# Performance work log

Hardware: AMD Instinct MI355X
Metric: run time of the kernel (lower is better)

Reference implementation:

```python
import jax, jax.numpy as jnp
import numpy as np

B, N, E = 32, 196, 512      # batch, image regions, encoder_dim
D, EMB, V = 512, 512, 32000  # decoder_dim, embedding_dim, vocab
MAXLEN = 65


def setup_inputs() -> dict:
    key = jax.random.key(0)
    ks = jax.random.split(key, 16)
    s = lambda *sh: 1.0 / np.sqrt(sh[-1])
    return {
        "image_features": jax.random.normal(ks[0], (B, N, E), jnp.float32),
        "captions": jax.random.randint(ks[1], (B, MAXLEN), 0, V),
        "emb": jax.random.normal(ks[2], (V, EMB), jnp.float32) * 0.02,
        "Wh0": jax.random.normal(ks[3], (D, E), jnp.float32) * s(E),
        "bh0": jnp.zeros((D,), jnp.float32),
        "Wc0": jax.random.normal(ks[4], (D, E), jnp.float32) * s(E),
        "bc0": jnp.zeros((D,), jnp.float32),
        "Wenc": jax.random.normal(ks[5], (D, E), jnp.float32) * s(E),
        "Wdec": jax.random.normal(ks[6], (D, D), jnp.float32) * s(D),
        "v_att": jax.random.normal(ks[7], (D,), jnp.float32) * s(D),
        "W_ih": jax.random.normal(ks[8], (4 * D, EMB + E), jnp.float32) * s(EMB + E),
        "b_ih": jnp.zeros((4 * D,), jnp.float32),
        "W_hh": jax.random.normal(ks[9], (4 * D, D), jnp.float32) * s(D),
        "b_hh": jnp.zeros((4 * D,), jnp.float32),
        "Wfc": jax.random.normal(ks[10], (V, D), jnp.float32) * s(D),
        "bfc": jnp.zeros((V,), jnp.float32),
    }


def reference(image_features, captions, emb, Wh0, bh0, Wc0, bc0,
              Wenc, Wdec, v_att, W_ih, b_ih, W_hh, b_hh, Wfc, bfc):
    seq_len = captions.shape[1] - 1
    emb_caps = emb[captions]                     # [B, maxlen, EMB]
    xs = jnp.swapaxes(emb_caps[:, :seq_len], 0, 1)  # [T, B, EMB]

    feat_mean = image_features.mean(axis=1)      # [B, E]
    h0 = feat_mean @ Wh0.T + bh0                 # [B, D]
    c0 = feat_mean @ Wc0.T + bc0
    feat_proj = jnp.einsum('bne,de->bnd', image_features, Wenc)  # [B, N, D]

    def step(carry, xt):
        h, c = carry
        # Bahdanau additive attention over the N image regions
        e = jnp.einsum('bnd,d->bn', jnp.tanh(feat_proj + (h @ Wdec.T)[:, None, :]), v_att)
        alpha = jax.nn.softmax(e, axis=-1)                       # [B, N]
        ctx = jnp.einsum('bn,bne->be', alpha, image_features)    # [B, E]
        x = jnp.concatenate([xt, ctx], axis=-1)                  # [B, EMB+E]
        gates = x @ W_ih.T + b_ih + h @ W_hh.T + b_hh            # [B, 4D]
        i, f, g, o = jnp.split(gates, 4, axis=-1)
        c_new = jax.nn.sigmoid(f) * c + jax.nn.sigmoid(i) * jnp.tanh(g)
        h_new = jax.nn.sigmoid(o) * jnp.tanh(c_new)
        out = h_new @ Wfc.T + bfc                                # [B, V]
        return (h_new, c_new), (out, alpha)
    # dropout_p=0.0 -> dropout is identity (eval-mode reference)
    _, (outs, alphas) = jax.lax.scan(step, (h0, c0), xs)
    outputs = jnp.swapaxes(outs, 0, 1)            # [B, T, V]
    attention_weights = jnp.swapaxes(alphas, 0, 1)  # [B, T, N]
    return outputs, attention_weights
```

## Files before the change

kernel.cpp:

```cpp
#include <hip/hip_runtime.h>
#include <cstdint>
#include <cstddef>

typedef _Float16 half2_t __attribute__((ext_vector_type(2)));
typedef _Float16 half4_t __attribute__((ext_vector_type(4)));
typedef _Float16 half8_t __attribute__((ext_vector_type(8)));
typedef float    float4_t __attribute__((ext_vector_type(4)));

#define CAPLEN 65
#define PTLD 200

#define AT_LD(p)     __hip_atomic_load((p), __ATOMIC_RELAXED, __HIP_MEMORY_SCOPE_AGENT)
#define AT_ST(p, v)  __hip_atomic_store((p), (v), __ATOMIC_RELAXED, __HIP_MEMORY_SCOPE_AGENT)

#if defined(__has_builtin)
#if __has_builtin(__builtin_amdgcn_fdot2)
#define HAS_FDOT2 1
#endif
#endif

__device__ __forceinline__ float fdot2f(half2_t a, half2_t b, float c) {
#ifdef HAS_FDOT2
  return __builtin_amdgcn_fdot2(a, b, c, false);
#else
  return c + (float)a[0]*(float)b[0] + (float)a[1]*(float)b[1];
#endif
}

__device__ __forceinline__ float fast_tanh(float x) {
  float e = __expf(2.f*x);
  return 1.f - 2.f/(e + 1.f);
}
__device__ __forceinline__ float fast_sig(float x) {
  return 1.f/(1.f + __expf(-x));
}

#define MS_C1 65536
#define MS_C2 131072
#define MS_C3 655360
#define MS_C4 917504
#define MS_C5 5013504
#define MS_C6 5816320
#define MS_C7 6078464
#define MS_C8 6078976
#define MS_C9 6087168
#define MS_C10 6218240

__device__ __forceinline__ void cvt_quad(const float* __restrict__ s,
                                         _Float16* __restrict__ d, int q) {
  float4 v = ((const float4*)s)[q];
  half4_t h;
  h[0] = (_Float16)v.x; h[1] = (_Float16)v.y; h[2] = (_Float16)v.z; h[3] = (_Float16)v.w;
  ((half4_t*)d)[q] = h;
}

__global__ void mega_setup_k(
    const float* __restrict__ Wenc, _Float16* __restrict__ Wenc_h,
    const float* __restrict__ Wdec, _Float16* __restrict__ Wdec_h,
    const float* __restrict__ Wih,  _Float16* __restrict__ Wih_h,
    const float* __restrict__ Whh,  _Float16* __restrict__ Whh_h,
    const float* __restrict__ Wfc,  _Float16* __restrict__ Wfc_h,
    const float* __restrict__ imgf, _Float16* __restrict__ imgf_h,
    const float* __restrict__ emb,  const int* __restrict__ cap,
    _Float16* __restrict__ X_h,
    const float* __restrict__ b_ih, const float* __restrict__ b_hh,
    float* __restrict__ bsum,
    unsigned long long* __restrict__ hpub64,
    unsigned long long* __restrict__ epub64) {
  int stride = gridDim.x*blockDim.x;
  for (int i = blockIdx.x*blockDim.x + threadIdx.x; i < MS_C10; i += stride) {
    if (i < MS_C1) {
      cvt_quad(Wenc, Wenc_h, i);
    } else if (i < MS_C2) {
      cvt_quad(Wdec, Wdec_h, i - MS_C1);
    } else if (i < MS_C3) {
      cvt_quad(Wih, Wih_h, i - MS_C2);
    } else if (i < MS_C4) {
      cvt_quad(Whh, Whh_h, i - MS_C3);
    } else if (i < MS_C5) {
      cvt_quad(Wfc, Wfc_h, i - MS_C4);
    } else if (i < MS_C6) {
      cvt_quad(imgf, imgf_h, i - MS_C5);
    } else if (i < MS_C7) {
      int g = i - MS_C6;
      int row = g >> 7, q = g & 127;
      int t = row >> 5, b = row & 31;
      int tok = cap[b*CAPLEN + t];
      float4 v = ((const float4*)(emb + (size_t)tok*512))[q];
      half4_t h;
      h[0] = (_Float16)v.x; h[1] = (_Float16)v.y; h[2] = (_Float16)v.z; h[3] = (_Float16)v.w;
      *(half4_t*)(X_h + (size_t)row*512 + q*4) = h;
    } else if (i < MS_C8) {
      int q = i - MS_C7;
      float4 a = ((const float4*)b_ih)[q];
      float4 b = ((const float4*)b_hh)[q];
      float4 o; o.x = a.x+b.x; o.y = a.y+b.y; o.z = a.z+b.z; o.w = a.w+b.w;
      ((float4*)bsum)[q] = o;
    } else if (i < MS_C9) {
      hpub64[8192 + (i - MS_C8)] = ~0ull;
    } else {
      epub64[i - MS_C9] = ~0ull;
    }
  }
}

__global__ void init_state_k(const float* __restrict__ imgf,
                             const float* __restrict__ Wh0, const float* __restrict__ bh0,
                             const float* __restrict__ Wc0, const float* __restrict__ bc0,
                             float* __restrict__ c_state,
                             unsigned long long* __restrict__ hpub64) {
  __shared__ float fm[512];
  __shared__ float hsh[512];
  int b = blockIdx.x, tid = threadIdx.x;
  for (int dI = tid; dI < 512; dI += 256) {
    float s = 0.f;
    const float* p = imgf + ((size_t)b*196)*512 + dI;
    for (int n = 0; n < 196; n++) s += p[(size_t)n*512];
    fm[dI] = s * (1.f/196.f);
  }
  __syncthreads();
  for (int dI = tid; dI < 512; dI += 256) {
    const float* wh = Wh0 + (size_t)dI*512;
    const float* wc = Wc0 + (size_t)dI*512;
    float h = bh0[dI], c = bc0[dI];
    for (int k = 0; k < 512; k++) { h += fm[k]*wh[k]; c += fm[k]*wc[k]; }
    hsh[dI] = h;
    c_state[b*512 + dI] = c;
  }
  __syncthreads();
  {
    half2_t h2; h2[0] = (_Float16)hsh[2*tid]; h2[1] = (_Float16)hsh[2*tid+1];
    union { half2_t h; unsigned u; } cv; cv.h = h2;
    hpub64[(size_t)b*256 + tid] = (unsigned long long)cv.u;
  }
}

__device__ __forceinline__ void gemm_pt_body(const _Float16* __restrict__ A, int lda,
    const _Float16* __restrict__ Bimg, _Float16* __restrict__ Cpt, int mrows,
    int bx, int by, int bz, int tid) {
  const _Float16* B = Bimg + (size_t)bz*196*512;
  _Float16* C = Cpt + (size_t)bz*mrows*PTLD;
  int wave = tid >> 6, lane = tid & 63;
  int m0 = by*128 + (wave >> 1)*64;
  int n0 = bx*128 + (wave & 1)*64;
  int lr = lane & 15, quad = lane >> 4;
  float4_t acc[4][4];
  #pragma unroll
  for (int i = 0; i < 4; i++)
    #pragma unroll
    for (int j = 0; j < 4; j++)
      acc[i][j] = (float4_t){0.f, 0.f, 0.f, 0.f};
  const _Float16* Ap = A + (size_t)(m0 + lr)*lda + quad*8;
  const _Float16* Bp = B + (size_t)(n0 + lr)*512 + quad*8;
  for (int k0 = 0; k0 < 512; k0 += 32) {
    half8_t af[4], bf[4];
    #pragma unroll
    for (int i = 0; i < 4; i++) af[i] = *(const half8_t*)(Ap + (size_t)i*16*lda + k0);
    #pragma unroll
    for (int i = 0; i < 4; i++) bf[i] = *(const half8_t*)(Bp + (size_t)i*16*512 + k0);
    #pragma unroll
    for (int mi = 0; mi < 4; mi++)
      #pragma unroll
      for (int ni = 0; ni < 4; ni++)
        acc[mi][ni] = __builtin_amdgcn_mfma_f32_16x16x32_f16(af[mi], bf[ni], acc[mi][ni], 0, 0, 0);
  }
  #pragma unroll
  for (int mi = 0; mi < 4; mi++) {
    #pragma unroll
    for (int ni = 0; ni < 4; ni++) {
      int col = n0 + ni*16 + lr;
      if (col < PTLD) {
        #pragma unroll
        for (int r = 0; r < 4; r++) {
          int row = m0 + mi*16 + quad*4 + r;
          C[(size_t)row*PTLD + col] = (_Float16)acc[mi][ni][r];
        }
      }
    }
  }
}

__device__ __forceinline__ void gemm_ab0_body(const _Float16* __restrict__ A, int lda,
    const _Float16* __restrict__ B, int ldb, float* __restrict__ C, int ldc,
    const float* __restrict__ bias, int K, int bx, int by, int tid) {
  int wave = tid >> 6, lane = tid & 63;
  int m0 = by*128 + (wave >> 1)*64;
  int n0 = bx*128 + (wave & 1)*64;
  int lr = lane & 15, quad = lane >> 4;
  float4_t acc[4][4];
  #pragma unroll
  for (int i = 0; i < 4; i++)
    #pragma unroll
    for (int j = 0; j < 4; j++)
      acc[i][j] = (float4_t){0.f, 0.f, 0.f, 0.f};
  const _Float16* Ap = A + (size_t)(m0 + lr)*lda + quad*8;
  const _Float16* Bp = B + (size_t)(n0 + lr)*ldb + quad*8;
  for (int k0 = 0; k0 < K; k0 += 32) {
    half8_t af[4], bf[4];
    #pragma unroll
    for (int i = 0; i < 4; i++) af[i] = *(const half8_t*)(Ap + (size_t)i*16*lda + k0);
    #pragma unroll
    for (int i = 0; i < 4; i++) bf[i] = *(const half8_t*)(Bp + (size_t)i*16*ldb + k0);
    #pragma unroll
    for (int mi = 0; mi < 4; mi++)
      #pragma unroll
      for (int ni = 0; ni < 4; ni++)
        acc[mi][ni] = __builtin_amdgcn_mfma_f32_16x16x32_f16(af[mi], bf[ni], acc[mi][ni], 0, 0, 0);
  }
  #pragma unroll
  for (int mi = 0; mi < 4; mi++) {
    #pragma unroll
    for (int ni = 0; ni < 4; ni++) {
      int col = n0 + ni*16 + lr;
      float bv = bias[col];
      #pragma unroll
      for (int r = 0; r < 4; r++) {
        int row = m0 + mi*16 + quad*4 + r;
        C[(size_t)row*ldc + col] = acc[mi][ni][r] + bv;
      }
    }
  }
}

__global__ void __launch_bounds__(256) setup_gemms_k(
    const _Float16* __restrict__ Wenc_h, const _Float16* __restrict__ Wih_h,
    const _Float16* __restrict__ imgf_h, const _Float16* __restrict__ X_h,
    _Float16* __restrict__ fproj_T, _Float16* __restrict__ P_T,
    float* __restrict__ Xg, const float* __restrict__ bsum) {
  int bid = blockIdx.x, tid = threadIdx.x;
  if (bid < 256) {
    gemm_pt_body(Wenc_h, 512, imgf_h, fproj_T, 512, bid & 1, (bid >> 1) & 3, bid >> 3, tid);
  } else if (bid < 1280) {
    int l = bid - 256;
    gemm_pt_body(Wih_h + 512, 1024, imgf_h, P_T, 2048, l & 1, (l >> 1) & 15, l >> 5, tid);
  } else {
    int l = bid - 1280;
    gemm_ab0_body(X_h, 512, Wih_h, 1024, Xg, 2048, bsum, 512, l & 15, l >> 4, tid);
  }
}

__global__ void __launch_bounds__(512) loop_k(
    const _Float16* __restrict__ Wdec_h,
    const _Float16* __restrict__ Whh_h,
    const _Float16* __restrict__ fproj_T,
    const _Float16* __restrict__ P_T,
    const float*    __restrict__ Xg,
    const float*    __restrict__ v_att,
    const float*    __restrict__ c_init,
    unsigned long long* __restrict__ hpub64,
    unsigned long long* __restrict__ epub64,
    _Float16*       __restrict__ H_h,
    float*          __restrict__ out_alpha)
{
  __shared__ _Float16 P_lds[98*256*2];
  __shared__ _Float16 fp_lds[64*PTLD];
  __shared__ __align__(16) unsigned hl_u[256];
  __shared__ _Float16 Hbuf[64*64];
  __shared__ float abuf[25*64];
  __shared__ float vlf[64];
  __shared__ float hwf[64];
  __shared__ float ep[2][256];
  __shared__ float redA[8];
  __shared__ float redB[8];
  __shared__ float sa[256];
  __shared__ float sm2[512];
  __shared__ float hnl[64];
  int bid = blockIdx.x, tid = threadIdx.x;
  int r = bid & 7, b = bid >> 3;
  int row = tid & 255, half = tid >> 8;
  int typ = row >> 6, dl = row & 63;
  int grow = typ*512 + r*64 + dl;
  int lane = tid & 63;

  if (tid < 64) vlf[tid] = v_att[r*64 + tid];
  float c_reg = (tid < 64) ? c_init[b*512 + r*64 + tid] : 0.f;

  if (tid < 256) {
    const _Float16* pp = P_T + ((size_t)b*2048 + grow)*PTLD;
    half2_t* P2 = (half2_t*)P_lds;
    for (int k8 = 0; k8 < 24; k8++) {
      half8_t v8 = *(const half8_t*)(pp + k8*8);
      #pragma unroll
      for (int j2 = 0; j2 < 4; j2++) {
        half2_t h2; h2[0] = v8[2*j2]; h2[1] = v8[2*j2+1];
        P2[(k8*4 + j2)*256 + row] = h2;
      }
    }
    half4_t v4 = *(const half4_t*)(pp + 192);
    half2_t a2; a2[0] = v4[0]; a2[1] = v4[1];
    half2_t b2; b2[0] = v4[2]; b2[1] = v4[3];
    P2[96*256 + row] = a2;
    P2[97*256 + row] = b2;
  } else {
    for (int i = tid - 256; i < 64*25; i += 256) {
      int d = i/25, c = i - d*25;
      *(half8_t*)(fp_lds + d*PTLD + c*8) =
        *(const half8_t*)(fproj_T + ((size_t)(b*512 + r*64 + d))*PTLD + c*8);
    }
  }
  int eBase = (r < 4) ? r*25 : 100 + (r-4)*24;
  int eCnt  = (r < 4) ? 25 : 24;

  for (int t = 0; t < 64; ++t) {
    if (tid < 256) {
      const unsigned long long* hp = hpub64 + ((size_t)(t & 1)*32 + b)*256 + tid;
      unsigned long long v = AT_LD(hp);
      while ((unsigned)(v >> 32) != (unsigned)t) {
        __builtin_amdgcn_s_sleep(1);
        v = AT_LD(hp);
      }
      hl_u[tid] = (unsigned)v;
    }
    float xg = (half == 1) ? Xg[((size_t)t*32 + b)*2048 + grow] : 0.f;
    __syncthreads();
    {
      int dim = tid >> 3, s = tid & 7;
      const half8_t* wr = (const half8_t*)(Wdec_h + (size_t)(r*64 + dim)*512 + s*64);
      const half8_t* hh = ((const half8_t*)(const _Float16*)hl_u) + s*8;
      float a = 0.f;
      #pragma unroll
      for (int k8 = 0; k8 < 8; k8++) {
        half8_t w8 = wr[k8]; half8_t h8 = hh[k8];
        const half2_t* wp = (const half2_t*)&w8;
        const half2_t* hp = (const half2_t*)&h8;
        a = fdot2f(wp[0], hp[0], a);
        a = fdot2f(wp[1], hp[1], a);
        a = fdot2f(wp[2], hp[2], a);
        a = fdot2f(wp[3], hp[3], a);
      }
      a += __shfl_xor(a, 1);
      a += __shfl_xor(a, 2);
      a += __shfl_xor(a, 4);
      if (s == 0) hwf[dim] = a;
    }
    __syncthreads();
    {
      float a = 0.f;
      if (row < 196) {
        #pragma unroll 8
        for (int j = 0; j < 32; j++) {
          int dd = half*32 + j;
          a += vlf[dd] * fast_tanh((float)fp_lds[dd*PTLD + row] + hwf[dd]);
        }
      }
      ep[half][row] = a;
    }
    __syncthreads();
    if (tid < 196) {
      union { float f; unsigned u; } c; c.f = ep[0][tid] + ep[1][tid];
      AT_ST(epub64 + (((size_t)(t & 1)*32 + b)*256 + tid)*8 + r,
            ((unsigned long long)(unsigned)t << 32) | (unsigned long long)c.u);
    }
    float gacc = xg;
    {
      const half8_t* wr = (const half8_t*)(Whh_h + (size_t)grow*512 + half*256);
      const half8_t* hh = ((const half8_t*)(const _Float16*)hl_u) + half*32;
      for (int k8 = 0; k8 < 32; k8++) {
        half8_t w8 = wr[k8]; half8_t h8 = hh[k8];
        const half2_t* wp = (const half2_t*)&w8;
        const half2_t* hp = (const half2_t*)&h8;
        gacc = fdot2f(wp[0], hp[0], gacc);
        gacc = fdot2f(wp[1], hp[1], gacc);
        gacc = fdot2f(wp[2], hp[2], gacc);
        gacc = fdot2f(wp[3], hp[3], gacc);
      }
    }
    float ee = -1e30f;
    if (tid < 196) {
      const unsigned long long* pb = epub64 + (((size_t)(t & 1)*32 + b)*256 + tid)*8;
      float vals[8];
      unsigned done = 0;
      while (done != 0xFFu) {
        #pragma unroll
        for (int rr = 0; rr < 8; rr++) {
          if (!(done & (1u << rr))) {
            unsigned long long v = AT_LD(pb + rr);
            if ((unsigned)(v >> 32) == (unsigned)t) {
              union { unsigned u; float f; } c; c.u = (unsigned)v;
              vals[rr] = c.f; done |= (1u << rr);
            }
          }
        }
        if (done != 0xFFu) __builtin_amdgcn_s_sleep(1);
      }
      ee = ((vals[0]+vals[1]) + (vals[2]+vals[3])) + ((vals[4]+vals[5]) + (vals[6]+vals[7]));
    }
    {
      float m = ee;
      #pragma unroll
      for (int off = 32; off > 0; off >>= 1) m = fmaxf(m, __shfl_xor(m, off));
      if (lane == 0) redA[tid >> 6] = m;
    }
    __syncthreads();
    float mx = redA[0];
    #pragma unroll
    for (int i = 1; i < 8; i++) mx = fmaxf(mx, redA[i]);
    float ex = (tid < 196) ? __expf(ee - mx) : 0.f;
    {
      float s = ex;
      #pragma unroll
      for (int off = 32; off > 0; off >>= 1) s += __shfl_xor(s, off);
      if (lane == 0) redB[tid >> 6] = s;
    }
    __syncthreads();
    float tot = redB[0];
    #pragma unroll
    for (int i = 1; i < 8; i++) tot += redB[i];
    float al = ex * (1.f/tot);
    if (tid < 256) sa[tid] = al;
    if (tid >= eBase && tid < eBase + eCnt)
      abuf[(tid - eBase)*64 + t] = al;
    __syncthreads();
    {
      const half2_t* P2 = (const half2_t*)P_lds;
      const float2*  sap = (const float2*)sa;
      int n2b = half*49;
      #pragma unroll 7
      for (int n2 = n2b; n2 < n2b + 49; n2++) {
        half2_t p = P2[n2*256 + row];
        float2 s2 = sap[n2];
        gacc += s2.x*(float)p[0] + s2.y*(float)p[1];
      }
      sm2[tid] = gacc;
    }
    __syncthreads();
    if (tid < 64) {
      float ig = sm2[tid]       + sm2[tid + 256];
      float fg = sm2[64 + tid]  + sm2[tid + 320];
      float gg = sm2[128 + tid] + sm2[tid + 384];
      float og = sm2[192 + tid] + sm2[tid + 448];
      float cn = fast_sig(fg)*c_reg + fast_sig(ig)*fast_tanh(gg);
      float hn = fast_sig(og)*fast_tanh(cn);
      c_reg = cn;
      hnl[tid] = hn;
      Hbuf[t*64 + tid] = (_Float16)hn;
    }
    __syncthreads();
    if (tid < 32) {
      half2_t h2; h2[0] = (_Float16)hnl[2*tid]; h2[1] = (_Float16)hnl[2*tid+1];
      union { half2_t h; unsigned u; } cv; cv.h = h2;
      AT_ST(hpub64 + ((size_t)((t + 1) & 1)*32 + b)*256 + r*32 + tid,
            ((unsigned long long)(unsigned)(t + 1) << 32) | (unsigned long long)cv.u);
    }
    __syncthreads();
  }

  for (int i = tid; i < 64*64; i += 512) {
    int t = i >> 6, d = i & 63;
    H_h[((size_t)t*32 + b)*512 + r*64 + d] = Hbuf[i];
  }
  for (int i = tid; i < eCnt*64; i += 512) {
    int ln = i >> 6, tt = i & 63;
    out_alpha[((size_t)b*64 + tt)*196 + eBase + ln] = abuf[ln*64 + tt];
  }
}

__global__ void __launch_bounds__(512) logits_k(const _Float16* __restrict__ A,
    const _Float16* __restrict__ Bw, float* __restrict__ C,
    const float* __restrict__ bias) {
  int wave = threadIdx.x >> 6, lane = threadIdx.x & 63;
  int lr = lane & 15, quad = lane >> 4;
  int waveM = wave >> 1, waveN = wave & 1;
  int n0 = blockIdx.x*128 + waveN*64;
  const _Float16* Bp = Bw + (size_t)(n0 + lr)*512 + quad*8;
  float bv[4];
  #pragma unroll
  for (int ni = 0; ni < 4; ni++) bv[ni] = bias[n0 + ni*16 + lr];
  for (int it = 0; it < 4; ++it) {
    int m0 = (blockIdx.y*16 + it*4 + waveM)*64;
    const _Float16* Ap = A + (size_t)(m0 + lr)*512 + quad*8;
    float4_t acc[4][4];
    #pragma unroll
    for (int i = 0; i < 4; i++)
      #pragma unroll
      for (int j = 0; j < 4; j++)
        acc[i][j] = (float4_t){0.f, 0.f, 0.f, 0.f};
    for (int k0 = 0; k0 < 512; k0 += 32) {
      half8_t af[4], bf[4];
      #pragma unroll
      for (int i = 0; i < 4; i++) af[i] = *(const half8_t*)(Ap + (size_t)i*16*512 + k0);
      #pragma unroll
      for (int i = 0; i < 4; i++) bf[i] = *(const half8_t*)(Bp + (size_t)i*16*512 + k0);
      #pragma unroll
      for (int mi = 0; mi < 4; mi++)
        #pragma unroll
        for (int ni = 0; ni < 4; ni++)
          acc[mi][ni] = __builtin_amdgcn_mfma_f32_16x16x32_f16(af[mi], bf[ni], acc[mi][ni], 0, 0, 0);
    }
    #pragma unroll
    for (int mi = 0; mi < 4; mi++) {
      #pragma unroll
      for (int ni = 0; ni < 4; ni++) {
        int col = n0 + ni*16 + lr;
        #pragma unroll
        for (int r = 0; r < 4; r++) {
          int row = m0 + mi*16 + quad*4 + r;
          size_t orow = (size_t)((row & 31)*64 + (row >> 5));
          __builtin_nontemporal_store(acc[mi][ni][r] + bv[ni], C + orow*32000 + col);
        }
      }
    }
  }
}

extern "C" void kernel_launch(void* const* d_in, const int* in_sizes, int n_in,
                              void* d_out, int out_size, void* d_ws, size_t ws_size,
                              hipStream_t stream) {
  const float* imgf  = (const float*)d_in[0];
  const int*   cap   = (const int*)d_in[1];
  const float* emb   = (const float*)d_in[2];
  const float* Wh0   = (const float*)d_in[3];
  const float* bh0   = (const float*)d_in[4];
  const float* Wc0   = (const float*)d_in[5];
  const float* bc0   = (const float*)d_in[6];
  const float* Wenc  = (const float*)d_in[7];
  const float* Wdec  = (const float*)d_in[8];
  const float* v_att = (const float*)d_in[9];
  const float* W_ih  = (const float*)d_in[10];
  const float* b_ih  = (const float*)d_in[11];
  const float* W_hh  = (const float*)d_in[12];
  const float* b_hh  = (const float*)d_in[13];
  const float* Wfc   = (const float*)d_in[14];
  const float* bfc   = (const float*)d_in[15];
  float* out = (float*)d_out;
  (void)in_sizes; (void)n_in; (void)out_size; (void)ws_size;

  char* ws = (char*)d_ws;
  size_t off = 0;
  auto alloc = [&](size_t bytes) -> void* {
    void* p = ws + off;
    off += (bytes + 255) & ~(size_t)255;
    return p;
  };
  _Float16* Wenc_h  = (_Float16*)alloc((size_t)512*512*2);
  _Float16* Wdec_h  = (_Float16*)alloc((size_t)512*512*2);
  _Float16* Wih_h   = (_Float16*)alloc((size_t)2048*1024*2);
  _Float16* Whh_h   = (_Float16*)alloc((size_t)2048*512*2);
  _Float16* Wfc_h   = (_Float16*)alloc((size_t)32000*512*2);
  _Float16* imgf_h  = (_Float16*)alloc((size_t)32*196*512*2);
  _Float16* fproj_T = (_Float16*)alloc((size_t)32*512*PTLD*2);
  _Float16* P_T     = (_Float16*)alloc((size_t)32*2048*PTLD*2);
  _Float16* X_h     = (_Float16*)alloc((size_t)64*32*512*2);
  float*    Xg      = (float*)alloc((size_t)64*32*2048*4);
  float*    bsum    = (float*)alloc((size_t)2048*4);
  float*    c_state = (float*)alloc((size_t)32*512*4);
  unsigned long long* hpub64 = (unsigned long long*)alloc((size_t)2*32*256*8);
  unsigned long long* epub64 = (unsigned long long*)alloc((size_t)2*32*256*8*8);
  _Float16* H_h     = (_Float16*)alloc((size_t)2048*512*2);

  mega_setup_k<<<dim3(2048), dim3(256), 0, stream>>>(
      Wenc, Wenc_h, Wdec, Wdec_h, W_ih, Wih_h, W_hh, Whh_h, Wfc, Wfc_h,
      imgf, imgf_h, emb, cap, X_h, b_ih, b_hh, bsum, hpub64, epub64);
  init_state_k<<<dim3(32), dim3(256), 0, stream>>>(imgf, Wh0, bh0, Wc0, bc0, c_state, hpub64);
  setup_gemms_k<<<dim3(1536), dim3(256), 0, stream>>>(
      Wenc_h, Wih_h, imgf_h, X_h, fproj_T, P_T, Xg, bsum);

  float* out_alpha = out + (size_t)32*64*32000;
  loop_k<<<dim3(256), dim3(512), 0, stream>>>(Wdec_h, Whh_h, fproj_T, P_T, Xg,
      v_att, c_state, hpub64, epub64, H_h, out_alpha);
  logits_k<<<dim3(250, 2), dim3(512), 0, stream>>>(H_h, Wfc_h, out, bfc);
}
```

Before: 1.941 ms.

## Publish partial h·Wdec instead of partial attention energies; recompute energies per block

Changes the split of attention work across the 8 blocks per batch row. Before, each block computed attention energies for its 64-dim slice and published partial energy sums. Now each block computes a partial h·Wdec^T product for all 512 dims from its own h slice, using Wdec held in registers, and publishes it. Each block then sums the 8 partials and computes the full 196-region energy itself, reading fproj from global memory in a new row-major layout. The aim is to cut one cross-block exchange and barrier from the per-step critical path. The cost is 8x redundant energy computation, global fproj reads every step, a larger publish buffer, and a remapped block-to-batch assignment.

```diff
diff --git a/kernel.cpp b/kernel.cpp
--- a/kernel.cpp
+++ b/kernel.cpp
@@ -66,7 +66,7 @@
     const float* __restrict__ b_ih, const float* __restrict__ b_hh,
     float* __restrict__ bsum,
     unsigned long long* __restrict__ hpub64,
-    unsigned long long* __restrict__ epub64) {
+    unsigned long long* __restrict__ hwpub64) {
   int stride = gridDim.x*blockDim.x;
   for (int i = blockIdx.x*blockDim.x + threadIdx.x; i < MS_C10; i += stride) {
     if (i < MS_C1) {
@@ -99,7 +99,7 @@
     } else if (i < MS_C9) {
       hpub64[8192 + (i - MS_C8)] = ~0ull;
     } else {
-      epub64[i - MS_C9] = ~0ull;
+      hwpub64[131072 + (i - MS_C9)] = ~0ull;
     }
   }
 }
@@ -107,8 +107,10 @@
 __global__ void init_state_k(const float* __restrict__ imgf,
                              const float* __restrict__ Wh0, const float* __restrict__ bh0,
                              const float* __restrict__ Wc0, const float* __restrict__ bc0,
+                             const float* __restrict__ Wdec,
                              float* __restrict__ c_state,
-                             unsigned long long* __restrict__ hpub64) {
+                             unsigned long long* __restrict__ hpub64,
+                             unsigned long long* __restrict__ hwpub64) {
   __shared__ float fm[512];
   __shared__ float hsh[512];
   int b = blockIdx.x, tid = threadIdx.x;
@@ -132,6 +134,16 @@
     half2_t h2; h2[0] = (_Float16)hsh[2*tid]; h2[1] = (_Float16)hsh[2*tid+1];
     union { half2_t h; unsigned u; } cv; cv.h = h2;
     hpub64[(size_t)b*256 + tid] = (unsigned long long)cv.u;
+  }
+  for (int d = tid; d < 512; d += 256) {
+    const float* wd = Wdec + (size_t)d*512;
+    float s = 0.f;
+    for (int k = 0; k < 512; k++) s += wd[k]*hsh[k];
+    union { float f; unsigned u; } cv; cv.f = s;
+    unsigned long long* base = hwpub64 + ((size_t)b*512 + d)*8;
+    base[0] = (unsigned long long)cv.u;
+    #pragma unroll
+    for (int rr = 1; rr < 8; rr++) base[rr] = 0ull;
   }
 }
 
@@ -180,6 +192,47 @@
   }
 }
 
+__device__ __forceinline__ void gemm_ab1_body(const _Float16* __restrict__ A, int lda,
+    const _Float16* __restrict__ B, int ldb, _Float16* __restrict__ C, int ldc,
+    int K, int bx, int by, int tid) {
+  int wave = tid >> 6, lane = tid & 63;
+  int m0 = by*128 + (wave >> 1)*64;
+  int n0 = bx*128 + (wave & 1)*64;
+  int lr = lane & 15, quad = lane >> 4;
+  float4_t acc[4][4];
+  #pragma unroll
+  for (int i = 0; i < 4; i++)
+    #pragma unroll
+    for (int j = 0; j < 4; j++)
+      acc[i][j] = (float4_t){0.f, 0.f, 0.f, 0.f};
+  const _Float16* Ap = A + (size_t)(m0 + lr)*lda + quad*8;
+  const _Float16* Bp = B + (size_t)(n0 + lr)*ldb + quad*8;
+  for (int k0 = 0; k0 < K; k0 += 32) {
+    half8_t af[4], bf[4];
+    #pragma unroll
+    for (int i = 0; i < 4; i++) af[i] = *(const half8_t*)(Ap + (size_t)i*16*lda + k0);
+    #pragma unroll
+    for (int i = 0; i < 4; i++) bf[i] = *(const half8_t*)(Bp + (size_t)i*16*ldb + k0);
+    #pragma unroll
+    for (int mi = 0; mi < 4; mi++)
+      #pragma unroll
+      for (int ni = 0; ni < 4; ni++)
+        acc[mi][ni] = __builtin_amdgcn_mfma_f32_16x16x32_f16(af[mi], bf[ni], acc[mi][ni], 0, 0, 0);
+  }
+  #pragma unroll
+  for (int mi = 0; mi < 4; mi++) {
+    #pragma unroll
+    for (int ni = 0; ni < 4; ni++) {
+      int col = n0 + ni*16 + lr;
+      #pragma unroll
+      for (int r = 0; r < 4; r++) {
+        int row = m0 + mi*16 + quad*4 + r;
+        C[(size_t)row*ldc + col] = (_Float16)acc[mi][ni][r];
+      }
+    }
+  }
+}
+
 __device__ __forceinline__ void gemm_ab0_body(const _Float16* __restrict__ A, int lda,
     const _Float16* __restrict__ B, int ldb, float* __restrict__ C, int ldc,
     const float* __restrict__ bias, int K, int bx, int by, int tid) {
@@ -225,16 +278,16 @@
 __global__ void __launch_bounds__(256) setup_gemms_k(
     const _Float16* __restrict__ Wenc_h, const _Float16* __restrict__ Wih_h,
     const _Float16* __restrict__ imgf_h, const _Float16* __restrict__ X_h,
-    _Float16* __restrict__ fproj_T, _Float16* __restrict__ P_T,
+    _Float16* __restrict__ fproj_h, _Float16* __restrict__ P_T,
     float* __restrict__ Xg, const float* __restrict__ bsum) {
   int bid = blockIdx.x, tid = threadIdx.x;
-  if (bid < 256) {
-    gemm_pt_body(Wenc_h, 512, imgf_h, fproj_T, 512, bid & 1, (bid >> 1) & 3, bid >> 3, tid);
-  } else if (bid < 1280) {
-    int l = bid - 256;
+  if (bid < 196) {
+    gemm_ab1_body(imgf_h, 512, Wenc_h, 512, fproj_h, 512, 512, bid & 3, bid >> 2, tid);
+  } else if (bid < 1220) {
+    int l = bid - 196;
     gemm_pt_body(Wih_h + 512, 1024, imgf_h, P_T, 2048, l & 1, (l >> 1) & 15, l >> 5, tid);
   } else {
-    int l = bid - 1280;
+    int l = bid - 1220;
     gemm_ab0_body(X_h, 512, Wih_h, 1024, Xg, 2048, bsum, 512, l & 15, l >> 4, tid);
   }
 }
@@ -242,38 +295,45 @@
 __global__ void __launch_bounds__(512) loop_k(
     const _Float16* __restrict__ Wdec_h,
     const _Float16* __restrict__ Whh_h,
-    const _Float16* __restrict__ fproj_T,
+    const _Float16* __restrict__ fproj_h,
     const _Float16* __restrict__ P_T,
     const float*    __restrict__ Xg,
     const float*    __restrict__ v_att,
     const float*    __restrict__ c_init,
     unsigned long long* __restrict__ hpub64,
-    unsigned long long* __restrict__ epub64,
+    unsigned long long* __restrict__ hwpub64,
     _Float16*       __restrict__ H_h,
     float*          __restrict__ out_alpha)
 {
   __shared__ _Float16 P_lds[98*256*2];
-  __shared__ _Float16 fp_lds[64*PTLD];
   __shared__ __align__(16) unsigned hl_u[256];
-  __shared__ _Float16 Hbuf[64*64];
-  __shared__ float abuf[25*64];
-  __shared__ float vlf[64];
-  __shared__ float hwf[64];
-  __shared__ float ep[2][256];
+  __shared__ float hwl[512];
+  __shared__ float vlf[512];
+  __shared__ float e_l[196];
   __shared__ float redA[8];
   __shared__ float redB[8];
   __shared__ float sa[256];
   __shared__ float sm2[512];
   __shared__ float hnl[64];
+  __shared__ _Float16 Hbuf[64*64];
+  __shared__ float abuf[25*64];
   int bid = blockIdx.x, tid = threadIdx.x;
-  int r = bid & 7, b = bid >> 3;
+  int r = (bid >> 3) & 7;
+  int b = (bid & 7) | ((bid >> 6) << 3);
   int row = tid & 255, half = tid >> 8;
   int typ = row >> 6, dl = row & 63;
   int grow = typ*512 + r*64 + dl;
   int lane = tid & 63;
 
-  if (tid < 64) vlf[tid] = v_att[r*64 + tid];
+  vlf[tid] = v_att[tid];
   float c_reg = (tid < 64) ? c_init[b*512 + r*64 + tid] : 0.f;
+
+  half8_t wdec_reg[8];
+  {
+    const half8_t* wp = (const half8_t*)(Wdec_h + (size_t)tid*512 + r*64);
+    #pragma unroll
+    for (int j = 0; j < 8; j++) wdec_reg[j] = wp[j];
+  }
 
   if (tid < 256) {
     const _Float16* pp = P_T + ((size_t)b*2048 + grow)*PTLD;
@@ -291,12 +351,6 @@
     half2_t b2; b2[0] = v4[2]; b2[1] = v4[3];
     P2[96*256 + row] = a2;
     P2[97*256 + row] = b2;
-  } else {
-    for (int i = tid - 256; i < 64*25; i += 256) {
-      int d = i/25, c = i - d*25;
-      *(half8_t*)(fp_lds + d*PTLD + c*8) =
-        *(const half8_t*)(fproj_T + ((size_t)(b*512 + r*64 + d))*PTLD + c*8);
-    }
   }
   int eBase = (r < 4) ? r*25 : 100 + (r-4)*24;
   int eCnt  = (r < 4) ? 25 : 24;
@@ -313,44 +367,6 @@
     }
     float xg = (half == 1) ? Xg[((size_t)t*32 + b)*2048 + grow] : 0.f;
     __syncthreads();
-    {
-      int dim = tid >> 3, s = tid & 7;
-      const half8_t* wr = (const half8_t*)(Wdec_h + (size_t)(r*64 + dim)*512 + s*64);
-      const half8_t* hh = ((const half8_t*)(const _Float16*)hl_u) + s*8;
-      float a = 0.f;
-      #pragma unroll
-      for (int k8 = 0; k8 < 8; k8++) {
-        half8_t w8 = wr[k8]; half8_t h8 = hh[k8];
-        const half2_t* wp = (const half2_t*)&w8;
-        const half2_t* hp = (const half2_t*)&h8;
-        a = fdot2f(wp[0], hp[0], a);
-        a = fdot2f(wp[1], hp[1], a);
-        a = fdot2f(wp[2], hp[2], a);
-        a = fdot2f(wp[3], hp[3], a);
-      }
-      a += __shfl_xor(a, 1);
-      a += __shfl_xor(a, 2);
-      a += __shfl_xor(a, 4);
-      if (s == 0) hwf[dim] = a;
-    }
-    __syncthreads();
-    {
-      float a = 0.f;
-      if (row < 196) {
-        #pragma unroll 8
-        for (int j = 0; j < 32; j++) {
-          int dd = half*32 + j;
-          a += vlf[dd] * fast_tanh((float)fp_lds[dd*PTLD + row] + hwf[dd]);
-        }
-      }
-      ep[half][row] = a;
-    }
-    __syncthreads();
-    if (tid < 196) {
-      union { float f; unsigned u; } c; c.f = ep[0][tid] + ep[1][tid];
-      AT_ST(epub64 + (((size_t)(t & 1)*32 + b)*256 + tid)*8 + r,
-            ((unsigned long long)(unsigned)t << 32) | (unsigned long long)c.u);
-    }
     float gacc = xg;
     {
       const half8_t* wr = (const half8_t*)(Whh_h + (size_t)grow*512 + half*256);
@@ -365,9 +381,8 @@
         gacc = fdot2f(wp[3], hp[3], gacc);
       }
     }
-    float ee = -1e30f;
-    if (tid < 196) {
-      const unsigned long long* pb = epub64 + (((size_t)(t & 1)*32 + b)*256 + tid)*8;
+    {
+      const unsigned long long* pb = hwpub64 + (((size_t)(t & 1)*32 + b)*512 + tid)*8;
       float vals[8];
       unsigned done = 0;
       while (done != 0xFFu) {
@@ -383,8 +398,28 @@
         }
         if (done != 0xFFu) __builtin_amdgcn_s_sleep(1);
       }
-      ee = ((vals[0]+vals[1]) + (vals[2]+vals[3])) + ((vals[4]+vals[5]) + (vals[6]+vals[7]));
-    }
+      hwl[tid] = ((vals[0]+vals[1]) + (vals[2]+vals[3]))
+               + ((vals[4]+vals[5]) + (vals[6]+vals[7]));
+    }
+    __syncthreads();
+    if (tid < 392) {
+      int n = tid >> 1, dh = tid & 1;
+      int base = dh << 8;
+      const half8_t* fp8 = (const half8_t*)(fproj_h + ((size_t)(b*196 + n))*512 + base);
+      float a = 0.f;
+      for (int k8 = 0; k8 < 32; k8++) {
+        half8_t f = fp8[k8];
+        #pragma unroll
+        for (int j = 0; j < 8; j++) {
+          int k = base + k8*8 + j;
+          a += vlf[k] * fast_tanh((float)f[j] + hwl[k]);
+        }
+      }
+      a += __shfl_xor(a, 1);
+      if (dh == 0) e_l[n] = a;
+    }
+    __syncthreads();
+    float ee = (tid < 196) ? e_l[tid] : -1e30f;
     {
       float m = ee;
       #pragma unroll
@@ -440,6 +475,18 @@
       half2_t h2; h2[0] = (_Float16)hnl[2*tid]; h2[1] = (_Float16)hnl[2*tid+1];
       union { half2_t h; unsigned u; } cv; cv.h = h2;
       AT_ST(hpub64 + ((size_t)((t + 1) & 1)*32 + b)*256 + r*32 + tid,
+            ((unsigned long long)(unsigned)(t + 1) << 32) | (unsigned long long)cv.u);
+    }
+    {
+      float a = 0.f;
+      #pragma unroll
+      for (int v = 0; v < 8; v++) {
+        half8_t w8 = wdec_reg[v];
+        #pragma unroll
+        for (int j = 0; j < 8; j++) a += (float)w8[j] * hnl[v*8 + j];
+      }
+      union { float f; unsigned u; } cv; cv.f = a;
+      AT_ST(hwpub64 + (((size_t)((t + 1) & 1)*32 + b)*512 + tid)*8 + r,
             ((unsigned long long)(unsigned)(t + 1) << 32) | (unsigned long long)cv.u);
     }
     __syncthreads();
@@ -538,25 +585,26 @@
   _Float16* Whh_h   = (_Float16*)alloc((size_t)2048*512*2);
   _Float16* Wfc_h   = (_Float16*)alloc((size_t)32000*512*2);
   _Float16* imgf_h  = (_Float16*)alloc((size_t)32*196*512*2);
-  _Float16* fproj_T = (_Float16*)alloc((size_t)32*512*PTLD*2);
+  _Float16* fproj_h = (_Float16*)alloc((size_t)32*196*512*2);
   _Float16* P_T     = (_Float16*)alloc((size_t)32*2048*PTLD*2);
   _Float16* X_h     = (_Float16*)alloc((size_t)64*32*512*2);
   float*    Xg      = (float*)alloc((size_t)64*32*2048*4);
   float*    bsum    = (float*)alloc((size_t)2048*4);
   float*    c_state = (float*)alloc((size_t)32*512*4);
-  unsigned long long* hpub64 = (unsigned long long*)alloc((size_t)2*32*256*8);
-  unsigned long long* epub64 = (unsigned long long*)alloc((size_t)2*32*256*8*8);
+  unsigned long long* hpub64  = (unsigned long long*)alloc((size_t)2*32*256*8);
+  unsigned long long* hwpub64 = (unsigned long long*)alloc((size_t)2*32*512*8*8);
   _Float16* H_h     = (_Float16*)alloc((size_t)2048*512*2);
 
   mega_setup_k<<<dim3(2048), dim3(256), 0, stream>>>(
       Wenc, Wenc_h, Wdec, Wdec_h, W_ih, Wih_h, W_hh, Whh_h, Wfc, Wfc_h,
-      imgf, imgf_h, emb, cap, X_h, b_ih, b_hh, bsum, hpub64, epub64);
-  init_state_k<<<dim3(32), dim3(256), 0, stream>>>(imgf, Wh0, bh0, Wc0, bc0, c_state, hpub64);
-  setup_gemms_k<<<dim3(1536), dim3(256), 0, stream>>>(
-      Wenc_h, Wih_h, imgf_h, X_h, fproj_T, P_T, Xg, bsum);
+      imgf, imgf_h, emb, cap, X_h, b_ih, b_hh, bsum, hpub64, hwpub64);
+  init_state_k<<<dim3(32), dim3(256), 0, stream>>>(imgf, Wh0, bh0, Wc0, bc0, Wdec,
+                                                   c_state, hpub64, hwpub64);
+  setup_gemms_k<<<dim3(1476), dim3(256), 0, stream>>>(
+      Wenc_h, Wih_h, imgf_h, X_h, fproj_h, P_T, Xg, bsum);
 
   float* out_alpha = out + (size_t)32*64*32000;
-  loop_k<<<dim3(256), dim3(512), 0, stream>>>(Wdec_h, Whh_h, fproj_T, P_T, Xg,
-      v_att, c_state, hpub64, epub64, H_h, out_alpha);
+  loop_k<<<dim3(256), dim3(512), 0, stream>>>(Wdec_h, Whh_h, fproj_h, P_T, Xg,
+      v_att, c_state, hpub64, hwpub64, H_h, out_alpha);
   logits_k<<<dim3(250, 2), dim3(512), 0, stream>>>(H_h, Wfc_h, out, bfc);
 }
```

Measured after the change: 3.772 ms. +94.3%, slower.
